# Performance work log

Hardware: AMD Instinct MI355X
Metric: run time of the kernel (lower is better)

Reference implementation:

```python
import jax, jax.numpy as jnp
import numpy as np
import random

NQUBIT = 4
NUM_CIRCUITS = 3
SEED = 1024
C64 = jnp.complex64

SINGLE = ['rx', 'ry', 'rz', 's', 't', 'p', 'u3']
DOUBLE = ['rxx', 'ryy', 'rzz', 'swap', 'cnot', 'cp', 'ch', 'cu', 'ct', 'cz']
PCOUNT = {'rx': 1, 'ry': 1, 'rz': 1, 's': 0, 't': 0, 'p': 1, 'u3': 3,
          'rxx': 1, 'ryy': 1, 'rzz': 1, 'swap': 0, 'cnot': 0, 'cp': 1,
          'ch': 0, 'cu': 3, 'ct': 0, 'cz': 0}


def build_circuits(nqubit=NQUBIT, num_circuits=NUM_CIRCUITS, seed=SEED):
    # Replays the torch module's python `random` stream (random.seed(seed))
    rng = random.Random(seed)
    circuits, off = [], 0
    for _ in range(num_circuits):
        gates = []
        for _blk in range(3):
            for i in range(nqubit):
                g = rng.choice(SINGLE)
                gates.append((g, (i,), off, PCOUNT[g])); off += PCOUNT[g]
            c, t = rng.sample(range(0, nqubit - 1), 2)
            g = rng.choice(DOUBLE)
            gates.append((g, (c, t), off, PCOUNT[g])); off += PCOUNT[g]
        circuits.append(gates)
    return circuits, off


def u3mat(th, ph, lam):
    c = jnp.cos(th * 0.5).astype(C64)
    s = jnp.sin(th * 0.5).astype(C64)
    eip = jnp.exp(1j * ph.astype(C64))
    eil = jnp.exp(1j * lam.astype(C64))
    return jnp.stack([jnp.stack([c, -eil * s]), jnp.stack([eip * s, eip * eil * c])])


def mat1(name, p):
    if name == 's':
        return jnp.array([[1, 0], [0, 1j]], C64)
    if name == 't':
        return jnp.array([[1, 0], [0, np.exp(1j * np.pi / 4)]], C64)
    if name == 'u3':
        return u3mat(p[0], p[1], p[2])
    one = jnp.ones((), C64); zero = jnp.zeros((), C64)
    if name == 'p':
        return jnp.stack([jnp.stack([one, zero]), jnp.stack([zero, jnp.exp(1j * p[0].astype(C64))])])
    h = p[0] * 0.5
    if name == 'rx':
        c = jnp.cos(h).astype(C64); s = (-1j * jnp.sin(h)).astype(C64)
        return jnp.stack([jnp.stack([c, s]), jnp.stack([s, c])])
    if name == 'ry':
        c = jnp.cos(h).astype(C64); s = jnp.sin(h).astype(C64)
        return jnp.stack([jnp.stack([c, -s]), jnp.stack([s, c])])
    if name == 'rz':
        e = jnp.exp(-1j * h.astype(C64))
        return jnp.stack([jnp.stack([e, zero]), jnp.stack([zero, jnp.conj(e)])])
    raise ValueError(name)


def mat2(name, p):
    if name == 'swap':
        return jnp.array([[1, 0, 0, 0], [0, 0, 1, 0], [0, 1, 0, 0], [0, 0, 0, 1]], C64)
    if name == 'cnot':
        return jnp.array([[1, 0, 0, 0], [0, 1, 0, 0], [0, 0, 0, 1], [0, 0, 1, 0]], C64)
    if name == 'cz':
        return jnp.diag(jnp.array([1, 1, 1, -1], C64))
    if name == 'ct':
        return jnp.diag(jnp.array([1, 1, 1, np.exp(1j * np.pi / 4)], C64))
    if name == 'ch':
        m = np.eye(4, dtype=np.complex64); r = 1.0 / np.sqrt(2.0)
        m[2:, 2:] = [[r, r], [r, -r]]
        return jnp.asarray(m)
    if name == 'cp':
        one = jnp.ones((), C64)
        return jnp.diag(jnp.stack([one, one, one, jnp.exp(1j * p[0].astype(C64))]))
    if name == 'cu':
        return jnp.zeros((4, 4), C64).at[:2, :2].set(jnp.eye(2, dtype=C64)).at[2:, 2:].set(u3mat(p[0], p[1], p[2]))
    h = p[0] * 0.5
    if name == 'rzz':
        e = jnp.exp(-1j * h.astype(C64)); ec = jnp.conj(e)
        return jnp.diag(jnp.stack([e, ec, ec, e]))
    if name == 'rxx':
        c = jnp.cos(h).astype(C64); s = (-1j * jnp.sin(h)).astype(C64)
        XX = jnp.array([[0, 0, 0, 1], [0, 0, 1, 0], [0, 1, 0, 0], [1, 0, 0, 0]], C64)
        return c * jnp.eye(4, dtype=C64) + s * XX
    if name == 'ryy':
        c = jnp.cos(h).astype(C64); s = (1j * jnp.sin(h)).astype(C64)
        YY = jnp.array([[0, 0, 0, 1], [0, 0, -1, 0], [0, -1, 0, 0], [1, 0, 0, 0]], C64)
        return c * jnp.eye(4, dtype=C64) + s * YY
    raise ValueError(name)


def apply1(state, U, q):
    # state: (N, 2,2,2,2); contract qubit-q axis with U
    state = jnp.moveaxis(state, 1 + q, -1)
    state = state @ U.T
    return jnp.moveaxis(state, -1, 1 + q)


def apply2(state, U, q0, q1):
    state = jnp.moveaxis(state, (1 + q0, 1 + q1), (-2, -1))
    sh = state.shape
    state = (state.reshape(sh[:-2] + (4,)) @ U.T).reshape(sh)
    return jnp.moveaxis(state, (-2, -1), (1 + q0, 1 + q1))


def zsigns(nqubit):
    idx = np.arange(2 ** nqubit)
    return np.stack([1.0 - 2.0 * ((idx >> (nqubit - 1 - q)) & 1) for q in range(nqubit)]).astype(np.float32)


def run_circuit(angles, params, gates, nqubit):
    N = angles.shape[0]
    h = angles * 0.5
    # rx(angle)|0> = [cos(a/2), -i sin(a/2)] per qubit -> product state (encode layer)
    v = jnp.stack([jnp.cos(h), -1j * jnp.sin(h)], axis=-1).astype(C64)  # (N, nq, 2)
    state = jnp.ones((N,), C64)
    for i in range(nqubit):
        state = state[..., None] * v[:, i].reshape((N,) + (1,) * i + (2,))
    for (name, qs, off, cnt) in gates:
        p = params[off:off + cnt]
        if len(qs) == 1:
            state = apply1(state, mat1(name, p), qs[0])
        else:
            state = apply2(state, mat2(name, p), qs[0], qs[1])
    probs = (state.real ** 2 + state.imag ** 2).reshape(N, -1)
    return probs @ jnp.asarray(zsigns(nqubit)).T  # (N, nqubit) Pauli-Z expectations


def _forward(x, params):
    B, C, H, W = x.shape
    circuits, _ = build_circuits()
    x_unf = jnp.moveaxis(x.reshape(B, C, H // 2, 2, W), 3, 4)  # torch unfold(2, 2, 2)
    xr = x_unf.reshape(-1, NQUBIT)
    exps = [run_circuit(xr, params, g, NQUBIT) for g in circuits]
    return jnp.stack(exps, axis=1).reshape(B, NUM_CIRCUITS, W, W)


def setup_inputs():
    key = jax.random.key(0)
    k1, k2 = jax.random.split(key)
    x = jax.random.normal(k1, (512, 1, 64, 64), jnp.float32)
    _, nparams = build_circuits()
    params = jax.random.uniform(k2, (nparams,), jnp.float32, -np.pi, np.pi)
    return {"x": x, "params": params}


def reference(x, params):
    return _forward(x, params)
```

## Files before the change

kernel.cpp:

```cpp
#include <hip/hip_runtime.h>
#include <stdint.h>


namespace {

typedef _Float16 half8 __attribute__((ext_vector_type(8)));
typedef float float4v __attribute__((ext_vector_type(4)));

struct GateList {
  int ty[45];
  int q0[45];
  int q1[45];
  int off[45];
};

struct PyRandom {
  uint32_t mt[624];
  int mti;
  void init_genrand(uint32_t s) {
    mt[0] = s;
    for (int i = 1; i < 624; ++i)
      mt[i] = 1812433253u * (mt[i - 1] ^ (mt[i - 1] >> 30)) + (uint32_t)i;
    mti = 624;
  }
  void init_by_array(const uint32_t* key, int klen) {
    init_genrand(19650218u);
    int i = 1, j = 0;
    int k = 624 > klen ? 624 : klen;
    for (; k; --k) {
      mt[i] = (mt[i] ^ ((mt[i - 1] ^ (mt[i - 1] >> 30)) * 1664525u)) + key[j] + (uint32_t)j;
      ++i; ++j;
      if (i >= 624) { mt[0] = mt[623]; i = 1; }
      if (j >= klen) j = 0;
    }
    for (k = 623; k; --k) {
      mt[i] = (mt[i] ^ ((mt[i - 1] ^ (mt[i - 1] >> 30)) * 1566083941u)) - (uint32_t)i;
      ++i;
      if (i >= 624) { mt[0] = mt[623]; i = 1; }
    }
    mt[0] = 0x80000000u;
    mti = 624;
  }
  uint32_t genrand() {
    if (mti >= 624) {
      const uint32_t mag[2] = {0u, 0x9908b0dfu};
      int kk; uint32_t y;
      for (kk = 0; kk < 227; ++kk) {
        y = (mt[kk] & 0x80000000u) | (mt[kk + 1] & 0x7fffffffu);
        mt[kk] = mt[kk + 397] ^ (y >> 1) ^ mag[y & 1];
      }
      for (; kk < 623; ++kk) {
        y = (mt[kk] & 0x80000000u) | (mt[kk + 1] & 0x7fffffffu);
        mt[kk] = mt[kk - 227] ^ (y >> 1) ^ mag[y & 1];
      }
      y = (mt[623] & 0x80000000u) | (mt[0] & 0x7fffffffu);
      mt[623] = mt[396] ^ (y >> 1) ^ mag[y & 1];
      mti = 0;
    }
    uint32_t y = mt[mti++];
    y ^= y >> 11;
    y ^= (y << 7) & 0x9d2c5680u;
    y ^= (y << 15) & 0xefc60000u;
    y ^= y >> 18;
    return y;
  }
  uint32_t getrandbits(int k) { return genrand() >> (32 - k); }
  uint32_t randbelow(uint32_t n) {
    int k = 32 - __builtin_clz(n);
    uint32_t r = getrandbits(k);
    while (r >= n) r = getrandbits(k);
    return r;
  }
};

void build_gatelist(GateList& gl) {
  PyRandom rng;
  uint32_t key = 1024u;
  rng.init_by_array(&key, 1);
  static const int PC_S[7]  = {1, 1, 1, 0, 0, 1, 3};
  static const int PC_D[10] = {1, 1, 1, 0, 0, 1, 0, 3, 0, 0};
  int off = 0, idx = 0;
  for (int circ = 0; circ < 3; ++circ) {
    for (int blk = 0; blk < 3; ++blk) {
      for (int i = 0; i < 4; ++i) {
        int g = (int)rng.randbelow(7);
        gl.ty[idx] = g; gl.q0[idx] = i; gl.q1[idx] = 0; gl.off[idx] = off;
        off += PC_S[g]; ++idx;
      }
      int pool[3] = {0, 1, 2};
      int j0 = (int)rng.randbelow(3); int c = pool[j0]; pool[j0] = pool[2];
      int j1 = (int)rng.randbelow(2); int t = pool[j1];
      int g = (int)rng.randbelow(10);
      gl.ty[idx] = 10 + g; gl.q0[idx] = c; gl.q1[idx] = t; gl.off[idx] = off;
      off += PC_D[g]; ++idx;
    }
  }
}

__device__ inline float2 cmul(float2 a, float2 b) {
  return make_float2(a.x * b.x - a.y * b.y, a.x * b.y + a.y * b.x);
}
__device__ inline float2 cadd(float2 a, float2 b) {
  return make_float2(a.x + b.x, a.y + b.y);
}
__device__ inline float2 shflx(float2 v, int m) {
  return make_float2(__shfl_xor(v.x, m), __shfl_xor(v.y, m));
}

__global__ __launch_bounds__(1024, 4) void qconv_fused(
    const float* __restrict__ x, const float* __restrict__ params,
    float* __restrict__ out, GateList gl) {
  __shared__ _Float16 ufrag[1536];
  __shared__ _Float16 lds[1024 * 24];

  const int tid  = threadIdx.x;
  const int wid  = tid >> 6;
  const int lane = tid & 63;
  const int quad = lane >> 4;
  const int n16  = lane & 15;
  const int rowbase = blockIdx.x * 1024 + wid * 64;
  const int r = rowbase + lane;

  const int b  = r >> 10;
  const int h2 = (r >> 5) & 31;
  const int j  = r & 31;
  const float* xb = x + b * 4096 + h2 * 128 + j * 2;
  float2 lo = *(const float2*)(xb);
  float2 hi = *(const float2*)(xb + 64);

  if (tid < 768) {
    const int circ = tid >> 8;
    const int col  = (tid >> 4) & 15;
    const int k    = tid & 15;

    float2 s = make_float2(k == col ? 1.f : 0.f, 0.f);

    for (int g = 0; g < 15; ++g) {
      int gi = circ * 15 + g;
      int ty = gl.ty[gi];
      int o  = gl.off[gi];
      if (ty < 7) {
        float2 G00 = make_float2(1, 0), G01 = make_float2(0, 0),
               G10 = make_float2(0, 0), G11 = make_float2(1, 0);
        if (ty == 0) {
          float c, sn; __sincosf(params[o] * 0.5f, &sn, &c);
          G00 = make_float2(c, 0); G01 = make_float2(0, -sn);
          G10 = make_float2(0, -sn); G11 = make_float2(c, 0);
        } else if (ty == 1) {
          float c, sn; __sincosf(params[o] * 0.5f, &sn, &c);
          G00 = make_float2(c, 0); G01 = make_float2(-sn, 0);
          G10 = make_float2(sn, 0); G11 = make_float2(c, 0);
        } else if (ty == 2) {
          float c, sn; __sincosf(params[o] * 0.5f, &sn, &c);
          G00 = make_float2(c, -sn); G11 = make_float2(c, sn);
        } else if (ty == 3) {
          G11 = make_float2(0, 1);
        } else if (ty == 4) {
          G11 = make_float2(0.7071067811865476f, 0.7071067811865476f);
        } else if (ty == 5) {
          float cp, sp; __sincosf(params[o], &sp, &cp);
          G11 = make_float2(cp, sp);
        } else {
          float th = params[o], phv = params[o + 1], lm = params[o + 2];
          float c, sn; __sincosf(th * 0.5f, &sn, &c);
          float cp, sp; __sincosf(phv, &sp, &cp);
          float cl, sl; __sincosf(lm, &sl, &cl);
          G00 = make_float2(c, 0);
          G01 = make_float2(-cl * sn, -sl * sn);
          G10 = make_float2(cp * sn, sp * sn);
          G11 = make_float2((cp * cl - sp * sl) * c, (cp * sl + sp * cl) * c);
        }
        int m = 1 << (3 - gl.q0[gi]);
        bool hib = (k & m) != 0;
        float2 p = shflx(s, m);
        float2 A = hib ? G11 : G00;
        float2 B = hib ? G10 : G01;
        s = cadd(cmul(A, s), cmul(B, p));
      } else {
        float2 G[4][4];
#pragma unroll
        for (int r2 = 0; r2 < 4; ++r2)
#pragma unroll
          for (int c2 = 0; c2 < 4; ++c2) G[r2][c2] = make_float2(0, 0);
        if (ty == 10) {
          float c, sn; __sincosf(params[o] * 0.5f, &sn, &c);
          G[0][0] = G[1][1] = G[2][2] = G[3][3] = make_float2(c, 0);
          G[0][3] = G[1][2] = G[2][1] = G[3][0] = make_float2(0, -sn);
        } else if (ty == 11) {
          float c, sn; __sincosf(params[o] * 0.5f, &sn, &c);
          G[0][0] = G[1][1] = G[2][2] = G[3][3] = make_float2(c, 0);
          G[0][3] = G[3][0] = make_float2(0, sn);
          G[1][2] = G[2][1] = make_float2(0, -sn);
        } else if (ty == 12) {
          float c, sn; __sincosf(params[o] * 0.5f, &sn, &c);
          G[0][0] = G[3][3] = make_float2(c, -sn);
          G[1][1] = G[2][2] = make_float2(c, sn);
        } else if (ty == 13) {
          G[0][0] = make_float2(1, 0); G[1][2] = make_float2(1, 0);
          G[2][1] = make_float2(1, 0); G[3][3] = make_float2(1, 0);
        } else if (ty == 14) {
          G[0][0] = G[1][1] = make_float2(1, 0);
          G[2][3] = G[3][2] = make_float2(1, 0);
        } else if (ty == 15) {
          G[0][0] = G[1][1] = G[2][2] = make_float2(1, 0);
          float cp, sp; __sincosf(params[o], &sp, &cp);
          G[3][3] = make_float2(cp, sp);
        } else if (ty == 16) {
          G[0][0] = G[1][1] = make_float2(1, 0);
          float rv = 0.7071067811865476f;
          G[2][2] = make_float2(rv, 0); G[2][3] = make_float2(rv, 0);
          G[3][2] = make_float2(rv, 0); G[3][3] = make_float2(-rv, 0);
        } else if (ty == 17) {
          G[0][0] = G[1][1] = make_float2(1, 0);
          float th = params[o], phv = params[o + 1], lm = params[o + 2];
          float c, sn; __sincosf(th * 0.5f, &sn, &c);
          float cp, sp; __sincosf(phv, &sp, &cp);
          float cl, sl; __sincosf(lm, &sl, &cl);
          G[2][2] = make_float2(c, 0);
          G[2][3] = make_float2(-cl * sn, -sl * sn);
          G[3][2] = make_float2(cp * sn, sp * sn);
          G[3][3] = make_float2((cp * cl - sp * sl) * c, (cp * sl + sp * cl) * c);
        } else if (ty == 18) {
          G[0][0] = G[1][1] = G[2][2] = make_float2(1, 0);
          G[3][3] = make_float2(0.7071067811865476f, 0.7071067811865476f);
        } else {
          G[0][0] = G[1][1] = G[2][2] = make_float2(1, 0);
          G[3][3] = make_float2(-1, 0);
        }
        int m0 = 1 << (3 - gl.q0[gi]);
        int m1 = 1 << (3 - gl.q1[gi]);
        bool b0 = (k & m0) != 0;
        bool b1 = (k & m1) != 0;
        float2 p0 = s;
        float2 p1 = shflx(s, m1);
        float2 p2 = shflx(s, m0);
        float2 p3 = shflx(s, m0 ^ m1);
        float2 acc = make_float2(0, 0);
#pragma unroll
        for (int jj = 0; jj < 4; ++jj) {
          float2 r0 = b1 ? G[1][1 ^ jj] : G[0][0 ^ jj];
          float2 r1 = b1 ? G[3][3 ^ jj] : G[2][2 ^ jj];
          float2 coef = b0 ? r1 : r0;
          float2 pj = (jj == 0) ? p0 : (jj == 1) ? p1 : (jj == 2) ? p2 : p3;
          acc = cadd(acc, cmul(coef, pj));
        }
        s = acc;
      }
    }

    int pc = __popc(col) & 3;
    float2 ph = make_float2(1, 0);
    if (pc == 1) ph = make_float2(0, -1);
    else if (pc == 2) ph = make_float2(-1, 0);
    else if (pc == 3) ph = make_float2(0, 1);
    float2 v = cmul(s, ph);

    int L = ((col >> 3) << 4) | k;
    int jf = col & 7;
    ufrag[((2 * circ) * 32 + L) * 8 + jf]     = (_Float16)v.x;
    ufrag[((2 * circ + 1) * 32 + L) * 8 + jf] = (_Float16)v.y;
  }

  float c0, s0, c1, s1, c2, s2, c3, s3;
  __sincosf(lo.x * 0.5f, &s0, &c0);
  __sincosf(hi.x * 0.5f, &s1, &c1);
  __sincosf(lo.y * 0.5f, &s2, &c2);
  __sincosf(hi.y * 0.5f, &s3, &c3);
  float t01[4] = {c0 * c1, c0 * s1, s0 * c1, s0 * s1};
  float t23[4] = {c2 * c3, c2 * s3, s2 * c3, s2 * s3};
  __align__(16) _Float16 rh[16];
#pragma unroll
  for (int a = 0; a < 4; ++a)
#pragma unroll
    for (int bq = 0; bq < 4; ++bq)
      rh[a * 4 + bq] = (_Float16)(t01[a] * t23[bq]);

  half8* dst = (half8*)&lds[tid * 24];
  dst[0] = *(const half8*)&rh[0];
  dst[1] = *(const half8*)&rh[8];

  __syncthreads();

  half8 af[6];
  if (lane < 32) {
    const half8* Uv = (const half8*)ufrag;
#pragma unroll
    for (int bb = 0; bb < 6; ++bb) af[bb] = Uv[bb * 32 + lane];
  } else {
#pragma unroll
    for (int bb = 0; bb < 6; ++bb)
#pragma unroll
      for (int e = 0; e < 8; ++e) af[bb][e] = (_Float16)0.f;
  }

#pragma unroll
  for (int t = 0; t < 4; ++t) {
    half8 bf;
    if (quad < 2) {
      bf = *(const half8*)&lds[(wid * 64 + t * 16 + n16) * 24 + quad * 8];
    } else {
#pragma unroll
      for (int e = 0; e < 8; ++e) bf[e] = (_Float16)0.f;
    }
    float4v acc[6];
#pragma unroll
    for (int bb = 0; bb < 6; ++bb) {
      float4v z = {0.f, 0.f, 0.f, 0.f};
      acc[bb] = __builtin_amdgcn_mfma_f32_16x16x32_f16(af[bb], bf, z, 0, 0, 0);
    }
    float4 E[3];
#pragma unroll
    for (int c = 0; c < 3; ++c) {
      float pv[4];
#pragma unroll
      for (int v = 0; v < 4; ++v) {
        float re = acc[2 * c][v], im = acc[2 * c + 1][v];
        pv[v] = fmaf(re, re, im * im);
      }
      float sA = pv[0] + pv[1], dA = pv[0] - pv[1];
      float sB = pv[2] + pv[3], dB = pv[2] - pv[3];
      float A00 = sA + sB;
      float A01 = dA + dB;
      float A10 = sA - sB;
      float r3 = A01 + __shfl_xor(A01, 16); r3 += __shfl_xor(r3, 32);
      float r2 = A10 + __shfl_xor(A10, 16); r2 += __shfl_xor(r2, 32);
      float h16v = __shfl_xor(A00, 16);
      float Ssum = A00 + h16v;
      float Dv = (quad & 1) ? (h16v - A00) : (A00 - h16v);
      float r1 = Dv + __shfl_xor(Dv, 32);
      float S32 = __shfl_xor(Ssum, 32);
      float r0 = (quad & 2) ? (S32 - Ssum) : (Ssum - S32);
      E[c] = make_float4(r0, r1, r2, r3);
    }
    if (quad < 3) {
      float4 ev = (quad == 0) ? E[0] : (quad == 1 ? E[1] : E[2]);
      int rowg = rowbase + t * 16 + n16;
      *(float4*)(out + (size_t)rowg * 12 + quad * 4) = ev;
    }
  }
}

}

extern "C" void kernel_launch(void* const* d_in, const int* in_sizes, int n_in,
                              void* d_out, int out_size, void* d_ws, size_t ws_size,
                              hipStream_t stream) {
  const float* x      = (const float*)d_in[0];
  const float* params = (const float*)d_in[1];
  float* out = (float*)d_out;
  (void)d_ws; (void)ws_size;

  GateList gl;
  build_gatelist(gl);

  int nrows = in_sizes[0] / 4;
  int grid  = nrows / 1024;
  hipLaunchKernelGGL(qconv_fused, dim3(grid), dim3(1024), 0, stream,
                     x, params, out, gl);
}
```

Measured before the change: 92.84 us.

## Precompute Pauli-Z observables as trig-basis tensor and reduce main kernel to one GEMM

```diff
diff --git a/kernel.cpp b/kernel.cpp
--- a/kernel.cpp
+++ b/kernel.cpp
@@ -107,28 +107,16 @@
   return make_float2(__shfl_xor(v.x, m), __shfl_xor(v.y, m));
 }
 
-__global__ __launch_bounds__(1024, 4) void qconv_fused(
-    const float* __restrict__ x, const float* __restrict__ params,
-    float* __restrict__ out, GateList gl) {
-  __shared__ _Float16 ufrag[1536];
-  __shared__ _Float16 lds[1024 * 24];
-
-  const int tid  = threadIdx.x;
-  const int wid  = tid >> 6;
-  const int lane = tid & 63;
-  const int quad = lane >> 4;
-  const int n16  = lane & 15;
-  const int rowbase = blockIdx.x * 1024 + wid * 64;
-  const int r = rowbase + lane;
-
-  const int b  = r >> 10;
-  const int h2 = (r >> 5) & 31;
-  const int j  = r & 31;
-  const float* xb = x + b * 4096 + h2 * 128 + j * 2;
-  float2 lo = *(const float2*)(xb);
-  float2 hi = *(const float2*)(xb + 64);
-
-  if (tid < 768) {
+__global__ __launch_bounds__(768) void build_T(
+    const float* __restrict__ params, _Float16* __restrict__ Tws, GateList gl) {
+  __shared__ float2 ldsU[768];
+  __shared__ float  ldsA[3072];
+
+  const int tid = threadIdx.x;
+
+  ((uint64_t*)Tws)[tid] = 0ull;
+
+  {
     const int circ = tid >> 8;
     const int col  = (tid >> 4) & 15;
     const int k    = tid & 15;
@@ -255,87 +243,139 @@
     else if (pc == 3) ph = make_float2(0, 1);
     float2 v = cmul(s, ph);
 
-    int L = ((col >> 3) << 4) | k;
-    int jf = col & 7;
-    ufrag[((2 * circ) * 32 + L) * 8 + jf]     = (_Float16)v.x;
-    ufrag[((2 * circ + 1) * 32 + L) * 8 + jf] = (_Float16)v.y;
-  }
-
+    ldsU[(circ * 16 + k) * 16 + col] = v;
+  }
+  __syncthreads();
+
+  {
+    const int circ = tid >> 8;
+    const int k    = (tid >> 4) & 15;
+    const int l    = tid & 15;
+    float a0 = 0.f, a1 = 0.f, a2 = 0.f, a3 = 0.f;
+    for (int i = 0; i < 16; ++i) {
+      float2 uk = ldsU[(circ * 16 + i) * 16 + k];
+      float2 ul = ldsU[(circ * 16 + i) * 16 + l];
+      float t = uk.x * ul.x + uk.y * ul.y;
+      a0 += (i & 8) ? -t : t;
+      a1 += (i & 4) ? -t : t;
+      a2 += (i & 2) ? -t : t;
+      a3 += (i & 1) ? -t : t;
+    }
+    ldsA[((circ * 4 + 0) * 16 + k) * 16 + l] = a0;
+    ldsA[((circ * 4 + 1) * 16 + k) * 16 + l] = a1;
+    ldsA[((circ * 4 + 2) * 16 + k) * 16 + l] = a2;
+    ldsA[((circ * 4 + 3) * 16 + k) * 16 + l] = a3;
+  }
+  __syncthreads();
+
+  for (int idx = tid; idx < 972; idx += 768) {
+    int cq = idx / 81;
+    int j  = idx - cq * 81;
+    int j0 = j / 27, j1 = (j / 9) % 3, j2 = (j % 9) / 3, j3 = j % 3;
+    int jarr[4] = {j0, j1, j2, j3};
+    float acc = 0.f;
+    for (int sel = 0; sel < 16; ++sel) {
+      int kk = 0, ll = 0;
+      float sg = 1.f;
+#pragma unroll
+      for (int q = 0; q < 4; ++q) {
+        int t = (sel >> (3 - q)) & 1;
+        kk |= t << (3 - q);
+        int lb = (jarr[q] == 2) ? (1 - t) : t;
+        ll |= lb << (3 - q);
+        if (jarr[q] == 1 && t) sg = -sg;
+      }
+      acc += sg * ldsA[(cq * 16 + kk) * 16 + ll];
+    }
+    float T = acc * 0.0625f;
+    _Float16 th = (_Float16)T;
+    _Float16 tl = (_Float16)(T - (float)th);
+    int mf = j >> 5, kkc = j & 31;
+    int L = ((kkc >> 3) << 4) | cq;
+    int jj = kkc & 7;
+    Tws[((mf * 2 + 0) * 64 + L) * 8 + jj] = th;
+    Tws[((mf * 2 + 1) * 64 + L) * 8 + jj] = tl;
+  }
+}
+
+__global__ __launch_bounds__(256, 3) void qconv_main(
+    const float* __restrict__ x, const _Float16* __restrict__ T,
+    float* __restrict__ out) {
+  __shared__ _Float16 lds[256 * 104];
+  const int tid  = threadIdx.x;
+  const int wid  = tid >> 6;
+  const int lane = tid & 63;
+  const int quad = lane >> 4;
+  const int n16  = lane & 15;
+  const int r = blockIdx.x * 256 + tid;
+
+  const half8* Tv = (const half8*)T;
+  half8 afh[3], afl[3];
+#pragma unroll
+  for (int mf = 0; mf < 3; ++mf) {
+    afh[mf] = Tv[(mf * 2 + 0) * 64 + lane];
+    afl[mf] = Tv[(mf * 2 + 1) * 64 + lane];
+  }
+
+  const int b  = r >> 10;
+  const int h2 = (r >> 5) & 31;
+  const int j  = r & 31;
+  const float* xb = x + b * 4096 + h2 * 128 + j * 2;
+  float2 lo = *(const float2*)(xb);
+  float2 hi = *(const float2*)(xb + 64);
   float c0, s0, c1, s1, c2, s2, c3, s3;
-  __sincosf(lo.x * 0.5f, &s0, &c0);
-  __sincosf(hi.x * 0.5f, &s1, &c1);
-  __sincosf(lo.y * 0.5f, &s2, &c2);
-  __sincosf(hi.y * 0.5f, &s3, &c3);
-  float t01[4] = {c0 * c1, c0 * s1, s0 * c1, s0 * s1};
-  float t23[4] = {c2 * c3, c2 * s3, s2 * c3, s2 * s3};
-  __align__(16) _Float16 rh[16];
-#pragma unroll
-  for (int a = 0; a < 4; ++a)
-#pragma unroll
-    for (int bq = 0; bq < 4; ++bq)
-      rh[a * 4 + bq] = (_Float16)(t01[a] * t23[bq]);
-
-  half8* dst = (half8*)&lds[tid * 24];
-  dst[0] = *(const half8*)&rh[0];
-  dst[1] = *(const half8*)&rh[8];
-
+  __sincosf(lo.x, &s0, &c0);
+  __sincosf(hi.x, &s1, &c1);
+  __sincosf(lo.y, &s2, &c2);
+  __sincosf(hi.y, &s3, &c3);
+  float f0[3] = {1.f, c0, s0}, f1[3] = {1.f, c1, s1};
+  float f2[3] = {1.f, c2, s2}, f3[3] = {1.f, c3, s3};
+  float g01e[11], g23[9];
+#pragma unroll
+  for (int a = 0; a < 9; ++a) g01e[a] = f0[a / 3] * f1[a % 3];
+  g01e[9] = 0.f; g01e[10] = 0.f;
+#pragma unroll
+  for (int bq = 0; bq < 9; ++bq) g23[bq] = f2[bq / 3] * f3[bq % 3];
+
+#pragma unroll
+  for (int w = 0; w < 12; ++w) {
+    __align__(16) _Float16 h8[8];
+#pragma unroll
+    for (int e = 0; e < 8; ++e) {
+      const int jg = w * 8 + e;
+      h8[e] = (_Float16)(g01e[jg / 9] * g23[jg % 9]);
+    }
+    *(half8*)&lds[tid * 104 + w * 8] = *(const half8*)h8;
+  }
   __syncthreads();
 
-  half8 af[6];
-  if (lane < 32) {
-    const half8* Uv = (const half8*)ufrag;
-#pragma unroll
-    for (int bb = 0; bb < 6; ++bb) af[bb] = Uv[bb * 32 + lane];
-  } else {
-#pragma unroll
-    for (int bb = 0; bb < 6; ++bb)
-#pragma unroll
-      for (int e = 0; e < 8; ++e) af[bb][e] = (_Float16)0.f;
-  }
-
+  half8 bf[4][3];
 #pragma unroll
   for (int t = 0; t < 4; ++t) {
-    half8 bf;
-    if (quad < 2) {
-      bf = *(const half8*)&lds[(wid * 64 + t * 16 + n16) * 24 + quad * 8];
-    } else {
-#pragma unroll
-      for (int e = 0; e < 8; ++e) bf[e] = (_Float16)0.f;
-    }
-    float4v acc[6];
-#pragma unroll
-    for (int bb = 0; bb < 6; ++bb) {
-      float4v z = {0.f, 0.f, 0.f, 0.f};
-      acc[bb] = __builtin_amdgcn_mfma_f32_16x16x32_f16(af[bb], bf, z, 0, 0, 0);
-    }
-    float4 E[3];
-#pragma unroll
-    for (int c = 0; c < 3; ++c) {
-      float pv[4];
-#pragma unroll
-      for (int v = 0; v < 4; ++v) {
-        float re = acc[2 * c][v], im = acc[2 * c + 1][v];
-        pv[v] = fmaf(re, re, im * im);
-      }
-      float sA = pv[0] + pv[1], dA = pv[0] - pv[1];
-      float sB = pv[2] + pv[3], dB = pv[2] - pv[3];
-      float A00 = sA + sB;
-      float A01 = dA + dB;
-      float A10 = sA - sB;
-      float r3 = A01 + __shfl_xor(A01, 16); r3 += __shfl_xor(r3, 32);
-      float r2 = A10 + __shfl_xor(A10, 16); r2 += __shfl_xor(r2, 32);
-      float h16v = __shfl_xor(A00, 16);
-      float Ssum = A00 + h16v;
-      float Dv = (quad & 1) ? (h16v - A00) : (A00 - h16v);
-      float r1 = Dv + __shfl_xor(Dv, 32);
-      float S32 = __shfl_xor(Ssum, 32);
-      float r0 = (quad & 2) ? (S32 - Ssum) : (Ssum - S32);
-      E[c] = make_float4(r0, r1, r2, r3);
-    }
-    if (quad < 3) {
-      float4 ev = (quad == 0) ? E[0] : (quad == 1 ? E[1] : E[2]);
-      int rowg = rowbase + t * 16 + n16;
-      *(float4*)(out + (size_t)rowg * 12 + quad * 4) = ev;
+    const int row = wid * 64 + t * 16 + n16;
+#pragma unroll
+    for (int mf = 0; mf < 3; ++mf)
+      bf[t][mf] = *(const half8*)&lds[row * 104 + mf * 32 + quad * 8];
+  }
+  float4v acc[4];
+#pragma unroll
+  for (int t = 0; t < 4; ++t) acc[t] = (float4v){0.f, 0.f, 0.f, 0.f};
+#pragma unroll
+  for (int mf = 0; mf < 3; ++mf) {
+#pragma unroll
+    for (int t = 0; t < 4; ++t)
+      acc[t] = __builtin_amdgcn_mfma_f32_16x16x32_f16(afl[mf], bf[t][mf], acc[t], 0, 0, 0);
+#pragma unroll
+    for (int t = 0; t < 4; ++t)
+      acc[t] = __builtin_amdgcn_mfma_f32_16x16x32_f16(afh[mf], bf[t][mf], acc[t], 0, 0, 0);
+  }
+
+  if (quad < 3) {
+#pragma unroll
+    for (int t = 0; t < 4; ++t) {
+      int rowg = blockIdx.x * 256 + wid * 64 + t * 16 + n16;
+      *(float4*)(out + (size_t)rowg * 12 + quad * 4) =
+          make_float4(acc[t][0], acc[t][1], acc[t][2], acc[t][3]);
     }
   }
 }
@@ -348,13 +388,15 @@
   const float* x      = (const float*)d_in[0];
   const float* params = (const float*)d_in[1];
   float* out = (float*)d_out;
-  (void)d_ws; (void)ws_size;
+  _Float16* Tws = (_Float16*)d_ws;
 
   GateList gl;
   build_gatelist(gl);
 
+  hipLaunchKernelGGL(build_T, dim3(1), dim3(768), 0, stream, params, Tws, gl);
+
   int nrows = in_sizes[0] / 4;
-  int grid  = nrows / 1024;
-  hipLaunchKernelGGL(qconv_fused, dim3(grid), dim3(1024), 0, stream,
-                     x, params, out, gl);
-}
+  int grid  = nrows / 256;
+  hipLaunchKernelGGL(qconv_main, dim3(grid), dim3(256), 0, stream,
+                     x, Tws, out);
+}
```

Measured after the change: 82.92 us. 10.7% less time.
